# Optimization experiments

Hardware: AMD Instinct MI355X
Metric: run time of the kernel (lower is better)

The kernel has to match this reference:

```python
import jax, jax.numpy as jnp
import numpy as np

N = 10000      # nodes
E = 160000     # edges (before self-loops)
H = 8          # heads
D_IN, D_H1, D_H2 = 165, 128, 1    # per-head channels of gat1 / gat2
HID = H * D_H1                    # 1024


def batchnorm(x, gamma, beta, eps=1e-5):
    # training-mode BatchNorm1d: biased batch statistics over the node axis
    mu = x.mean(0)
    var = x.var(0)
    return (x - mu) * jax.lax.rsqrt(var + eps) * gamma + beta


def gatv2(x, src, dst, Wl, bl, Wr, br, att, bias, heads, out_ch, concat, n_nodes):
    # PyG GATv2Conv: lin_l on source, lin_r on target; e = att . LeakyReLU(xl_j + xr_i)
    xl = (x @ Wl + bl).reshape(n_nodes, heads, out_ch)   # source transform
    xr = (x @ Wr + br).reshape(n_nodes, heads, out_ch)   # target transform
    e = jax.nn.leaky_relu(xl[src] + xr[dst], 0.2)        # [E,H,C]
    logits = jnp.einsum('ehc,hc->eh', e, att)            # [E,H]
    # segment softmax over incoming edges of each destination node
    m = jax.lax.stop_gradient(jax.ops.segment_max(logits, dst, num_segments=n_nodes))
    a = jnp.exp(logits - m[dst])
    s = jax.ops.segment_sum(a, dst, num_segments=n_nodes)
    alpha = a / (s[dst] + 1e-16)                          # [E,H]
    out = jax.ops.segment_sum(xl[src] * alpha[..., None], dst, num_segments=n_nodes)
    out = out.reshape(n_nodes, heads * out_ch) if concat else out.mean(1)
    return out + bias


def setup_inputs() -> dict:
    key = jax.random.key(0)
    ks = jax.random.split(key, 12)
    g = lambda k, shape, fan_in: jax.random.normal(k, shape, jnp.float32) * (1.0 / np.sqrt(fan_in))
    return {
        'x': jax.random.normal(ks[0], (N, D_IN), jnp.float32),
        'gamma1': jnp.ones((D_IN,), jnp.float32),
        'beta1': jnp.zeros((D_IN,), jnp.float32),
        'Wl1': g(ks[1], (D_IN, HID), D_IN),
        'bl1': jnp.zeros((HID,), jnp.float32),
        'Wr1': g(ks[2], (D_IN, HID), D_IN),
        'br1': jnp.zeros((HID,), jnp.float32),
        'att1': g(ks[3], (H, D_H1), D_H1),
        'bias1': jnp.zeros((HID,), jnp.float32),
        'gamma2': jnp.ones((HID,), jnp.float32),
        'beta2': jnp.zeros((HID,), jnp.float32),
        'Wl2': g(ks[4], (HID, H * D_H2), HID),
        'bl2': jnp.zeros((H * D_H2,), jnp.float32),
        'Wr2': g(ks[5], (HID, H * D_H2), HID),
        'br2': jnp.zeros((H * D_H2,), jnp.float32),
        'att2': g(ks[6], (H, D_H2), D_H2),
        'bias2': jnp.zeros((D_H2,), jnp.float32),
        'edge_index': jax.random.randint(ks[7], (2, E), 0, N, jnp.int64 if jax.config.jax_enable_x64 else jnp.int32),
    }


def reference(x, gamma1, beta1, Wl1, bl1, Wr1, br1, att1, bias1,
              gamma2, beta2, Wl2, bl2, Wr2, br2, att2, bias2, edge_index):
    loops = jnp.arange(N, dtype=edge_index.dtype)
    src = jnp.concatenate([edge_index[0], loops])   # add_self_loops=True (PyG default)
    dst = jnp.concatenate([edge_index[1], loops])
    h = batchnorm(x, gamma1, beta1)
    h = gatv2(h, src, dst, Wl1, bl1, Wr1, br1, att1, bias1, H, D_H1, True, N)
    h = batchnorm(h, gamma2, beta2)
    h = jax.nn.leaky_relu(h, 0.01)                  # F.leaky_relu default slope
    out = gatv2(h, src, dst, Wl2, bl2, Wr2, br2, att2, bias2, H, D_H2, False, N)
    return out
```

## Files before the change

kernel.cpp:

```cpp
#include <hip/hip_runtime.h>

#define NN   10000
#define E0   160000
#define ET   170000
#define DIN  165
#define KP   192
#define HID  1024
#define NH   8
#define BP   200
#define K2P  1032


typedef __bf16 bf16x8 __attribute__((ext_vector_type(8)));
typedef float  f32x4  __attribute__((ext_vector_type(4)));
typedef float  f32x2  __attribute__((ext_vector_type(2)));

__device__ __forceinline__ float bf2f(unsigned short u) {
    unsigned int i = ((unsigned int)u) << 16;
    return __builtin_bit_cast(float, i);
}
__device__ __forceinline__ unsigned short f2bf(float f) {
    unsigned int i = __builtin_bit_cast(unsigned int, f);
    i += 0x7fffu + ((i >> 16) & 1u);
    return (unsigned short)(i >> 16);
}
__device__ __forceinline__ float fin(float x) {
    return fminf(fmaxf(x, -1e30f), 1e30f);
}
__device__ __forceinline__ int clampi(int s) {
    return min(max(s, 0), NN - 1);
}
__device__ __forceinline__ void unpack8(uint4 u, float* f) {
    f[0]=bf2f((unsigned short)(u.x)); f[1]=bf2f((unsigned short)(u.x>>16));
    f[2]=bf2f((unsigned short)(u.y)); f[3]=bf2f((unsigned short)(u.y>>16));
    f[4]=bf2f((unsigned short)(u.z)); f[5]=bf2f((unsigned short)(u.z>>16));
    f[6]=bf2f((unsigned short)(u.w)); f[7]=bf2f((unsigned short)(u.w>>16));
}
__device__ __forceinline__ f32x2 up2(unsigned int u) {
    f32x2 r;
    r.x = __builtin_bit_cast(float, u << 16);
    r.y = __builtin_bit_cast(float, u & 0xffff0000u);
    return r;
}

__global__ __launch_bounds__(256) void debug_fill(float* __restrict__ out, float val) {
    int i = blockIdx.x * 256 + threadIdx.x;
    if (i < NN) out[i] = val;
}

__global__ __launch_bounds__(256) void bn1_stats(const float* __restrict__ x,
                                                 float* __restrict__ colsum, float* __restrict__ colsq) {
    int r0 = blockIdx.x * 125;
    int c = threadIdx.x;
    if (c >= DIN) return;
    float acc = 0.f, sq = 0.f;
    for (int r = r0; r < r0 + 125; ++r) {
        float v = x[(size_t)r * DIN + c];
        acc += v; sq += v * v;
    }
    atomicAdd(&colsum[c], acc);
    atomicAdd(&colsq[c], sq);
}

__global__ __launch_bounds__(256) void bn1_apply(const float* __restrict__ x,
                                                 const float* __restrict__ colsum, const float* __restrict__ colsq,
                                                 const float* __restrict__ gamma, const float* __restrict__ beta,
                                                 unsigned short* __restrict__ hn) {
    int idx = blockIdx.x * 256 + threadIdx.x;
    if (idx >= NN * KP) return;
    int r = idx / KP, c = idx - r * KP;
    float v = 0.f;
    if (c < DIN) {
        float mu  = colsum[c] * (1.f / NN);
        float var = fmaxf(colsq[c] * (1.f / NN) - mu * mu, 0.f);
        float a = gamma[c] * rsqrtf(var + 1e-5f);
        float b = beta[c] - mu * a;
        v = fin(x[(size_t)r * DIN + c] * a + b);
    }
    hn[idx] = f2bf(v);
}

__global__ __launch_bounds__(256) void w1_transpose(const float* __restrict__ wl,
                                                    const float* __restrict__ wr,
                                                    unsigned short* __restrict__ wlt,
                                                    unsigned short* __restrict__ wrt) {
    const float* src    = blockIdx.z ? wr  : wl;
    unsigned short* dst = blockIdx.z ? wrt : wlt;
    __shared__ float ts[32][65];
    const int k0 = blockIdx.x * 32;
    const int n0 = blockIdx.y * 64;
    const int tid = threadIdx.x;
    for (int idx = tid; idx < 32 * 64; idx += 256) {
        int k = idx >> 6, n = idx & 63;
        ts[k][n] = (k0 + k < DIN) ? src[(size_t)(k0 + k) * HID + n0 + n] : 0.f;
    }
    __syncthreads();
    for (int idx = tid; idx < 64 * 32; idx += 256) {
        int n = idx >> 5, k = idx & 31;
        dst[(size_t)(n0 + n) * KP + k0 + k] = f2bf(ts[k][n]);
    }
}

__global__ __launch_bounds__(256) void gemm1_kernel(
    const unsigned short* __restrict__ hn,
    const unsigned short* __restrict__ wlt,
    const unsigned short* __restrict__ wrt,
    const float* __restrict__ bl,
    const float* __restrict__ br,
    unsigned short* __restrict__ xl,
    unsigned short* __restrict__ xr) {
    __shared__ unsigned short bs[2][64 * BP];
    const int tid  = threadIdx.x;
    const int lane = tid & 63;
    const int wave = tid >> 6;
    const int col  = lane & 15;
    const int q    = lane >> 4;
    const int n0   = blockIdx.y * 64;

    for (int idx = tid; idx < 64 * 48 * 2; idx += 256) {
        int z = idx >= 64 * 48;
        int rem = z ? idx - 64 * 48 : idx;
        int r = rem / 48, c = rem - r * 48;
        const unsigned short* wt = z ? wrt : wlt;
        uint2 v = *(const uint2*)(wt + (size_t)(n0 + r) * KP + c * 4);
        *(uint2*)&bs[z][r * BP + c * 4] = v;
    }
    __syncthreads();

    const int mbase = blockIdx.x * 128 + wave * 32;
    const int am0 = mbase + col;
    const int am1 = am0 + 16;
    const bool aok0 = (am0 < NN), aok1 = (am1 < NN);

    f32x4 accL[2][4], accR[2][4];
    #pragma unroll
    for (int m = 0; m < 2; ++m)
        for (int nt = 0; nt < 4; ++nt)
            for (int r = 0; r < 4; ++r) { accL[m][nt][r] = 0.f; accR[m][nt][r] = 0.f; }

    #pragma unroll
    for (int kt = 0; kt < 6; ++kt) {
        const int kk = kt * 32 + q * 8;
        uint4 a0u = make_uint4(0u,0u,0u,0u), a1u = make_uint4(0u,0u,0u,0u);
        if (aok0) a0u = *(const uint4*)(hn + (size_t)am0 * KP + kk);
        if (aok1) a1u = *(const uint4*)(hn + (size_t)am1 * KP + kk);
        bf16x8 a0 = __builtin_bit_cast(bf16x8, a0u);
        bf16x8 a1 = __builtin_bit_cast(bf16x8, a1u);
        #pragma unroll
        for (int nt = 0; nt < 4; ++nt) {
            bf16x8 bfl = __builtin_bit_cast(bf16x8, *(const uint4*)&bs[0][(nt * 16 + col) * BP + kk]);
            accL[0][nt] = __builtin_amdgcn_mfma_f32_16x16x32_bf16(a0, bfl, accL[0][nt], 0, 0, 0);
            accL[1][nt] = __builtin_amdgcn_mfma_f32_16x16x32_bf16(a1, bfl, accL[1][nt], 0, 0, 0);
            bf16x8 bfr = __builtin_bit_cast(bf16x8, *(const uint4*)&bs[1][(nt * 16 + col) * BP + kk]);
            accR[0][nt] = __builtin_amdgcn_mfma_f32_16x16x32_bf16(a0, bfr, accR[0][nt], 0, 0, 0);
            accR[1][nt] = __builtin_amdgcn_mfma_f32_16x16x32_bf16(a1, bfr, accR[1][nt], 0, 0, 0);
        }
    }

    #pragma unroll
    for (int nt = 0; nt < 4; ++nt) {
        const int nc = n0 + nt * 16 + col;
        const float bLv = bl[nc];
        const float bRv = br[nc];
        #pragma unroll
        for (int m = 0; m < 2; ++m) {
            #pragma unroll
            for (int r = 0; r < 4; ++r) {
                const int row = mbase + m * 16 + q * 4 + r;
                if (row < NN) {
                    xl[(size_t)row * HID + nc] = f2bf(fin(accL[m][nt][r] + bLv));
                    xr[(size_t)row * HID + nc] = f2bf(fin(accR[m][nt][r] + bRv));
                }
            }
        }
    }
}

__global__ __launch_bounds__(256) void edge_hist(const int* __restrict__ ei, int* __restrict__ deg) {
    int e = blockIdx.x * 256 + threadIdx.x;
    if (e >= ET) return;
    int d = (e < E0) ? ei[E0 + e] : (e - E0);
    atomicAdd(&deg[clampi(d)], 1);
}

__global__ __launch_bounds__(1024) void scan_kernel(const int* __restrict__ deg,
                                                    int* __restrict__ offs, int* __restrict__ cur,
                                                    int* __restrict__ perm) {
    __shared__ int wsum[16];
    __shared__ int bins[64];
    __shared__ int bcur[64];
    const int tid = threadIdx.x;
    const int base = tid * 10;
    int loc[10];
    int run = 0;
    #pragma unroll
    for (int j = 0; j < 10; ++j) {
        int idx = base + j;
        int v = (idx < NN) ? deg[idx] : 0;
        loc[j] = run;
        run += v;
    }
    const int lane = tid & 63;
    const int w = tid >> 6;
    int inc = run;
    #pragma unroll
    for (int s = 1; s < 64; s <<= 1) {
        int t = __shfl_up(inc, s);
        if (lane >= s) inc += t;
    }
    if (lane == 63) wsum[w] = inc;
    if (tid < 64) bins[tid] = 0;
    __syncthreads();
    int woff = 0;
    #pragma unroll
    for (int k = 0; k < 16; ++k) woff += (k < w) ? wsum[k] : 0;
    const int toff = woff + inc - run;
    #pragma unroll
    for (int j = 0; j < 10; ++j) {
        int idx = base + j;
        if (idx < NN) {
            int e = toff + loc[j]; offs[idx] = e; cur[idx] = e;
            atomicAdd(&bins[63 - min(deg[idx], 63)], 1);
        }
    }
    if (tid == 1023) offs[NN] = woff + inc;
    __syncthreads();
    if (tid < 64) {
        int v = bins[tid];
        int binc = v;
        #pragma unroll
        for (int s = 1; s < 64; s <<= 1) {
            int t = __shfl_up(binc, s);
            if (tid >= s) binc += t;
        }
        bcur[tid] = binc - v;
    }
    __syncthreads();
    #pragma unroll
    for (int j = 0; j < 10; ++j) {
        int idx = base + j;
        if (idx < NN) {
            int pos = atomicAdd(&bcur[63 - min(deg[idx], 63)], 1);
            perm[pos] = idx;
        }
    }
}

__global__ __launch_bounds__(256) void edge_scatter(const int* __restrict__ ei,
                                                    int* __restrict__ cur, int* __restrict__ ssrc) {
    int e = blockIdx.x * 256 + threadIdx.x;
    if (e >= ET) return;
    int s, d;
    if (e < E0) { s = ei[e]; d = ei[E0 + e]; }
    else        { s = e - E0; d = e - E0; }
    int pos = atomicAdd(&cur[clampi(d)], 1);
    if (pos >= 0 && pos < ET) ssrc[pos] = clampi(s);
}

__global__ __launch_bounds__(256) void gat1_node(
    const unsigned short* __restrict__ xl1, const unsigned short* xr1,
    const float* __restrict__ att1, const float* __restrict__ bias1,
    const int* __restrict__ offs, const int* __restrict__ ssrc,
    const int* __restrict__ perm,
    unsigned short* agg) {
    const int lane = threadIdx.x & 63;
    const int wave = threadIdx.x >> 6;
    const int i = perm[blockIdx.x * 4 + wave];
    const int e0 = offs[i];
    const int e1 = max(offs[i + 1], e0 + 1);

    f32x2 xr2[8], at2[8], o2[8];
    {
        const uint4* xp = (const uint4*)(xr1 + (size_t)i * HID + lane * 16);
        uint4 u0 = xp[0], u1 = xp[1];
        unsigned int w[8] = {u0.x, u0.y, u0.z, u0.w, u1.x, u1.y, u1.z, u1.w};
        const float4* ap = (const float4*)(att1 + lane * 16);
        float4 a0 = ap[0], a1 = ap[1], a2 = ap[2], a3 = ap[3];
        float af[16] = {a0.x,a0.y,a0.z,a0.w, a1.x,a1.y,a1.z,a1.w,
                        a2.x,a2.y,a2.z,a2.w, a3.x,a3.y,a3.z,a3.w};
        #pragma unroll
        for (int j = 0; j < 8; ++j) {
            xr2[j] = up2(w[j]);
            at2[j].x = af[2*j]; at2[j].y = af[2*j+1];
            o2[j].x = 0.f; o2[j].y = 0.f;
        }
    }
    float s = 0.f;

    auto lded = [&](int e, uint4& u0, uint4& u1) {
        int ee = min(e, e1 - 1);
        int sidx = clampi(ssrc[ee]);
        const uint4* xp = (const uint4*)(xl1 + (size_t)sidx * HID + lane * 16);
        u0 = xp[0]; u1 = xp[1];
    };
    auto logit = [&](const uint4& u0, const uint4& u1) -> float {
        unsigned int w[8] = {u0.x, u0.y, u0.z, u0.w, u1.x, u1.y, u1.z, u1.w};
        f32x2 p = {0.f, 0.f}, q = {0.f, 0.f};
        #pragma unroll
        for (int j = 0; j < 8; j += 2) {
            f32x2 v0 = up2(w[j])     + xr2[j];
            f32x2 v1 = up2(w[j + 1]) + xr2[j + 1];
            p = __builtin_elementwise_fma(at2[j],     __builtin_elementwise_max(v0, 0.2f * v0), p);
            q = __builtin_elementwise_fma(at2[j + 1], __builtin_elementwise_max(v1, 0.2f * v1), q);
        }
        p += q;
        float r = p.x + p.y;
        r += __shfl_xor(r, 1); r += __shfl_xor(r, 2); r += __shfl_xor(r, 4);
        return __expf(fminf(r, 50.f));
    };
    auto accum = [&](const uint4& u0, const uint4& u1, float a) {
        unsigned int w[8] = {u0.x, u0.y, u0.z, u0.w, u1.x, u1.y, u1.z, u1.w};
        f32x2 av = {a, a};
        #pragma unroll
        for (int j = 0; j < 8; ++j)
            o2[j] = __builtin_elementwise_fma(av, up2(w[j]), o2[j]);
    };

    uint4 a0, a1, b0, b1, n0, n1, n2, n3;
    lded(e0,     a0, a1);
    lded(e0 + 1, b0, b1);
    int e = e0;
    while (e + 1 < e1) {
        lded(e + 2, n0, n1);
        lded(e + 3, n2, n3);
        float aa0 = logit(a0, a1);
        float aa1 = logit(b0, b1);
        s += aa0 + aa1;
        accum(a0, a1, aa0);
        accum(b0, b1, aa1);
        a0 = n0; a1 = n1; b0 = n2; b1 = n3;
        e += 2;
    }
    if (e < e1) {
        float aa = logit(a0, a1);
        s += aa;
        accum(a0, a1, aa);
    }

    const float inv = 1.f / (s + 1e-16f);
    const float4* bp = (const float4*)(bias1 + lane * 16);
    float4 bq0 = bp[0], bq1 = bp[1], bq2 = bp[2], bq3 = bp[3];
    float bb[16] = {bq0.x,bq0.y,bq0.z,bq0.w, bq1.x,bq1.y,bq1.z,bq1.w,
                    bq2.x,bq2.y,bq2.z,bq2.w, bq3.x,bq3.y,bq3.z,bq3.w};
    unsigned short ov[16];
    #pragma unroll
    for (int j = 0; j < 8; ++j) {
        ov[2*j]   = f2bf(fin(o2[j].x * inv + bb[2*j]));
        ov[2*j+1] = f2bf(fin(o2[j].y * inv + bb[2*j+1]));
    }
    uint4* op = (uint4*)(agg + (size_t)i * HID + lane * 16);
    op[0] = *(const uint4*)&ov[0];
    op[1] = *(const uint4*)&ov[8];
}

__global__ __launch_bounds__(256) void bn2_stats(const unsigned short* __restrict__ agg,
                                                 float* __restrict__ colsum, float* __restrict__ colsq) {
    int r0 = blockIdx.x * 125;
    int t = threadIdx.x;
    float s0=0,s1=0,s2=0,s3=0,q0=0,q1=0,q2=0,q3=0;
    for (int r = r0; r < r0 + 125; ++r) {
        const ushort4 u = *(const ushort4*)(agg + (size_t)r * HID + t * 4);
        float v0=bf2f(u.x), v1=bf2f(u.y), v2=bf2f(u.z), v3=bf2f(u.w);
        s0+=v0; q0+=v0*v0; s1+=v1; q1+=v1*v1;
        s2+=v2; q2+=v2*v2; s3+=v3; q3+=v3*v3;
    }
    atomicAdd(&colsum[t*4+0], s0); atomicAdd(&colsq[t*4+0], q0);
    atomicAdd(&colsum[t*4+1], s1); atomicAdd(&colsq[t*4+1], q1);
    atomicAdd(&colsum[t*4+2], s2); atomicAdd(&colsq[t*4+2], q2);
    atomicAdd(&colsum[t*4+3], s3); atomicAdd(&colsq[t*4+3], q3);
}

__global__ __launch_bounds__(256) void gemm2_kernel(
    const unsigned short* __restrict__ agg,
    const float* __restrict__ colsum, const float* __restrict__ colsq,
    const float* __restrict__ gamma, const float* __restrict__ beta,
    const float* __restrict__ wl2, const float* __restrict__ wr2,
    const float* __restrict__ bl2, const float* __restrict__ br2,
    float* __restrict__ xl2, float* __restrict__ xr2) {
    __shared__ unsigned short bs[16 * K2P];
    __shared__ float a2s[HID], b2s[HID];
    const int tid  = threadIdx.x;
    const int lane = tid & 63;
    const int wave = tid >> 6;
    const int col  = lane & 15;
    const int q    = lane >> 4;

    for (int idx = tid; idx < 16 * HID; idx += 256) {
        int n = idx >> 10, k = idx & (HID - 1);
        float v = (n < 8) ? wl2[k * 8 + n] : wr2[k * 8 + (n - 8)];
        bs[n * K2P + k] = f2bf(v);
    }
    for (int c = tid; c < HID; c += 256) {
        float mu  = colsum[c] * (1.f / NN);
        float var = fmaxf(colsq[c] * (1.f / NN) - mu * mu, 0.f);
        float a = gamma[c] * rsqrtf(var + 1e-5f);
        a2s[c] = a; b2s[c] = beta[c] - mu * a;
    }
    __syncthreads();

    const int mtile = blockIdx.x * 4 + wave;
    if (mtile >= NN / 16) return;
    const int m0 = mtile * 16;
    const int am = m0 + col;

    f32x4 acc;
    acc[0] = acc[1] = acc[2] = acc[3] = 0.f;
    #pragma unroll
    for (int kt = 0; kt < 32; ++kt) {
        const int kk = kt * 32 + q * 8;
        uint4 u = *(const uint4*)(agg + (size_t)am * HID + kk);
        float xv[8];
        unpack8(u, xv);
        unsigned short hv[8];
        #pragma unroll
        for (int j = 0; j < 8; ++j) {
            float v = xv[j] * a2s[kk + j] + b2s[kk + j];
            v = fmaxf(v, 0.01f * v);
            hv[j] = f2bf(fin(v));
        }
        bf16x8 af = __builtin_bit_cast(bf16x8, *(const uint4*)hv);
        bf16x8 bf = __builtin_bit_cast(bf16x8, *(const uint4*)&bs[col * K2P + kk]);
        acc = __builtin_amdgcn_mfma_f32_16x16x32_bf16(af, bf, acc, 0, 0, 0);
    }

    const float bv = (col < 8) ? bl2[col] : br2[col - 8];
    float* outp = (col < 8) ? (xl2 + col) : (xr2 + (col - 8));
    #pragma unroll
    for (int r = 0; r < 4; ++r) {
        const int row = m0 + q * 4 + r;
        outp[row * 8] = fin(acc[r] + bv);
    }
}

__global__ __launch_bounds__(256) void gat2_node(
    const float* __restrict__ xl2, const float* __restrict__ xr2,
    const float* __restrict__ att2, const float* __restrict__ bias2,
    const int* __restrict__ offs, const int* __restrict__ ssrc,
    const int* __restrict__ perm,
    float* __restrict__ out) {
    const int lane = threadIdx.x & 63;
    const int wave = threadIdx.x >> 6;
    const int i = perm[blockIdx.x * 4 + wave];
    const int h = lane & 7, slot = lane >> 3;
    const int e0 = offs[i];
    const int e1 = max(offs[i + 1], e0);
    const float xr_h = xr2[i * 8 + h];
    const float att_h = att2[h];
    float ssum = 0.f, wsum = 0.f;
    for (int eb = e0; eb < e1; eb += 8) {
        int e = eb + slot;
        if (e < e1) {
            float xlv = xl2[clampi(ssrc[e]) * 8 + h];
            float v = xlv + xr_h;
            v = fmaxf(v, 0.2f * v);
            float a = __expf(fminf(fin(att_h * v), 50.f));
            ssum += a; wsum += a * xlv;
        }
    }
    ssum += __shfl_xor(ssum, 8); ssum += __shfl_xor(ssum, 16); ssum += __shfl_xor(ssum, 32);
    wsum += __shfl_xor(wsum, 8); wsum += __shfl_xor(wsum, 16); wsum += __shfl_xor(wsum, 32);
    float v = fin(wsum / (ssum + 1e-16f));
    v += __shfl_xor(v, 1); v += __shfl_xor(v, 2); v += __shfl_xor(v, 4);
    if (lane == 0) out[i] = fin(v * 0.125f + bias2[0]);
}

extern "C" void kernel_launch(void* const* d_in, const int* in_sizes, int n_in,
                              void* d_out, int out_size, void* d_ws, size_t ws_size,
                              hipStream_t stream) {
    float* out = (float*)d_out;

    static const int expected[18] = {
        NN * DIN, DIN, DIN, DIN * HID, HID, DIN * HID, HID, HID, HID,
        HID, HID, HID * NH, NH, HID * NH, NH, NH, 1, 2 * E0
    };
    if (n_in != 18) {
        debug_fill<<<(NN + 255) / 256, 256, 0, stream>>>(out, 8192.f + 64.f * (float)n_in);
        return;
    }
    for (int i = 0; i < 18; ++i) {
        if (in_sizes[i] != expected[i]) {
            debug_fill<<<(NN + 255) / 256, 256, 0, stream>>>(out, 4096.f + 32.f * (float)i);
            return;
        }
    }

    const float* x      = (const float*)d_in[0];
    const float* gamma1 = (const float*)d_in[1];
    const float* beta1  = (const float*)d_in[2];
    const float* Wl1    = (const float*)d_in[3];
    const float* bl1    = (const float*)d_in[4];
    const float* Wr1    = (const float*)d_in[5];
    const float* br1    = (const float*)d_in[6];
    const float* att1   = (const float*)d_in[7];
    const float* bias1  = (const float*)d_in[8];
    const float* gamma2 = (const float*)d_in[9];
    const float* beta2  = (const float*)d_in[10];
    const float* Wl2    = (const float*)d_in[11];
    const float* bl2    = (const float*)d_in[12];
    const float* Wr2    = (const float*)d_in[13];
    const float* br2    = (const float*)d_in[14];
    const float* att2   = (const float*)d_in[15];
    const float* bias2  = (const float*)d_in[16];
    const int*   ei     = (const int*)d_in[17];

    char* p = (char*)d_ws;
    auto alloc = [&](size_t bytes) -> void* {
        void* r = (void*)p;
        p += (bytes + 255) & ~(size_t)255;
        return r;
    };
    unsigned short* xl1  = (unsigned short*)alloc((size_t)NN * HID * 2);
    unsigned short* xr1  = (unsigned short*)alloc((size_t)NN * HID * 2);
    unsigned short* agg  = xr1;
    unsigned short* hn   = (unsigned short*)alloc((size_t)NN * KP * 2);
    unsigned short* wlt  = (unsigned short*)alloc((size_t)HID * KP * 2);
    unsigned short* wrt  = (unsigned short*)alloc((size_t)HID * KP * 2);
    float*          xl2  = (float*)alloc((size_t)NN * 8 * 4);
    float*          xr2  = (float*)alloc((size_t)NN * 8 * 4);
    int*            offs = (int*)alloc((NN + 1) * 4);
    int*            cur  = (int*)alloc(NN * 4);
    int*            ssrc = (int*)alloc(ET * 4);
    int*            perm = (int*)alloc(NN * 4);
    char* zbase = p;
    float* colsum1 = (float*)alloc(DIN * 4);
    float* colsq1  = (float*)alloc(DIN * 4);
    float* colsum2 = (float*)alloc(HID * 4);
    float* colsq2  = (float*)alloc(HID * 4);
    int*   deg     = (int*)alloc(NN * 4);
    size_t zlen = (size_t)(p - zbase);
    hipMemsetAsync(zbase, 0, zlen, stream);

    bn1_stats<<<80, 256, 0, stream>>>(x, colsum1, colsq1);
    bn1_apply<<<(NN * KP + 255) / 256, 256, 0, stream>>>(x, colsum1, colsq1, gamma1, beta1, hn);
    w1_transpose<<<dim3(6, 16, 2), 256, 0, stream>>>(Wl1, Wr1, wlt, wrt);
    gemm1_kernel<<<dim3((NN + 127) / 128, HID / 64), 256, 0, stream>>>(hn, wlt, wrt, bl1, br1, xl1, xr1);
    edge_hist<<<(ET + 255) / 256, 256, 0, stream>>>(ei, deg);
    scan_kernel<<<1, 1024, 0, stream>>>(deg, offs, cur, perm);
    edge_scatter<<<(ET + 255) / 256, 256, 0, stream>>>(ei, cur, ssrc);
    gat1_node<<<NN / 4, 256, 0, stream>>>(xl1, xr1, att1, bias1, offs, ssrc, perm, agg);
    bn2_stats<<<80, 256, 0, stream>>>(agg, colsum2, colsq2);
    gemm2_kernel<<<(NN / 16 + 3) / 4, 256, 0, stream>>>(agg, colsum2, colsq2, gamma2, beta2,
                                                        Wl2, Wr2, bl2, br2, xl2, xr2);
    gat2_node<<<NN / 4, 256, 0, stream>>>(xl2, xr2, att2, bias2, offs, ssrc, perm, out);
}
```

Measured before the change: 278.9 us.

## Split GAT1 aggregation per head, stage GEMM1 stores in LDS, split-K GEMM2

The GAT1 node kernel now launches one block per (node group, head). Each wave handles a single node's head and processes four edges at once in 16-lane groups, with a cross-group shuffle reduction at the end. This raises parallelism and lowers per-thread register use compared with one wave per node over all 1024 channels. GEMM1's epilogue writes results to LDS and then issues coalesced 16-byte global stores instead of scattered 2-byte stores. GEMM2 splits K across the four waves of a block, reduces through shared memory, and launches four times as many blocks. The trade-offs are redundant index and offset loads per head, added shuffles, and more blocks.

```diff
diff --git a/kernel.cpp b/kernel.cpp
--- a/kernel.cpp
+++ b/kernel.cpp
@@ -157,6 +157,9 @@
         }
     }
 
+    __syncthreads();
+    unsigned short* cl = &bs[0][0];
+    unsigned short* cr = cl + 128 * 72;
     #pragma unroll
     for (int nt = 0; nt < 4; ++nt) {
         const int nc = n0 + nt * 16 + col;
@@ -166,12 +169,20 @@
         for (int m = 0; m < 2; ++m) {
             #pragma unroll
             for (int r = 0; r < 4; ++r) {
-                const int row = mbase + m * 16 + q * 4 + r;
-                if (row < NN) {
-                    xl[(size_t)row * HID + nc] = f2bf(fin(accL[m][nt][r] + bLv));
-                    xr[(size_t)row * HID + nc] = f2bf(fin(accR[m][nt][r] + bRv));
-                }
+                const int lrow = wave * 32 + m * 16 + q * 4 + r;
+                cl[lrow * 72 + nt * 16 + col] = f2bf(fin(accL[m][nt][r] + bLv));
+                cr[lrow * 72 + nt * 16 + col] = f2bf(fin(accR[m][nt][r] + bRv));
             }
+        }
+    }
+    __syncthreads();
+    const int mblk = blockIdx.x * 128;
+    for (int t = tid; t < 128 * 8; t += 256) {
+        const int row = t >> 3, ch = t & 7;
+        const int grow = mblk + row;
+        if (grow < NN) {
+            *(uint4*)(xl + (size_t)grow * HID + n0 + ch * 8) = *(const uint4*)&cl[row * 72 + ch * 8];
+            *(uint4*)(xr + (size_t)grow * HID + n0 + ch * 8) = *(const uint4*)&cr[row * 72 + ch * 8];
         }
     }
 }
@@ -264,93 +275,78 @@
     const int* __restrict__ perm,
     unsigned short* agg) {
     const int lane = threadIdx.x & 63;
-    const int wave = threadIdx.x >> 6;
-    const int i = perm[blockIdx.x * 4 + wave];
+    const int wv   = threadIdx.x >> 6;
+    const int h    = blockIdx.x & 7;
+    const int grp  = blockIdx.x >> 3;
+    const int i    = perm[grp * 4 + wv];
     const int e0 = offs[i];
     const int e1 = max(offs[i + 1], e0 + 1);
-
-    f32x2 xr2[8], at2[8], o2[8];
+    const int g = lane >> 4;
+    const int c = lane & 15;
+    const int hb = h * 128;
+
+    f32x2 xr20, xr21, xr22, xr23, at20, at21, at22, at23;
     {
-        const uint4* xp = (const uint4*)(xr1 + (size_t)i * HID + lane * 16);
-        uint4 u0 = xp[0], u1 = xp[1];
-        unsigned int w[8] = {u0.x, u0.y, u0.z, u0.w, u1.x, u1.y, u1.z, u1.w};
-        const float4* ap = (const float4*)(att1 + lane * 16);
-        float4 a0 = ap[0], a1 = ap[1], a2 = ap[2], a3 = ap[3];
-        float af[16] = {a0.x,a0.y,a0.z,a0.w, a1.x,a1.y,a1.z,a1.w,
-                        a2.x,a2.y,a2.z,a2.w, a3.x,a3.y,a3.z,a3.w};
-        #pragma unroll
-        for (int j = 0; j < 8; ++j) {
-            xr2[j] = up2(w[j]);
-            at2[j].x = af[2*j]; at2[j].y = af[2*j+1];
-            o2[j].x = 0.f; o2[j].y = 0.f;
-        }
-    }
+        uint4 u = *(const uint4*)(xr1 + (size_t)i * HID + hb + c * 8);
+        xr20 = up2(u.x); xr21 = up2(u.y); xr22 = up2(u.z); xr23 = up2(u.w);
+        float4 a0 = *(const float4*)(att1 + hb + c * 8);
+        float4 a1 = *(const float4*)(att1 + hb + c * 8 + 4);
+        at20.x=a0.x; at20.y=a0.y; at21.x=a0.z; at21.y=a0.w;
+        at22.x=a1.x; at22.y=a1.y; at23.x=a1.z; at23.y=a1.w;
+    }
+    f32x2 o20={0.f,0.f}, o21={0.f,0.f}, o22={0.f,0.f}, o23={0.f,0.f};
     float s = 0.f;
 
-    auto lded = [&](int e, uint4& u0, uint4& u1) {
-        int ee = min(e, e1 - 1);
-        int sidx = clampi(ssrc[ee]);
-        const uint4* xp = (const uint4*)(xl1 + (size_t)sidx * HID + lane * 16);
-        u0 = xp[0]; u1 = xp[1];
-    };
-    auto logit = [&](const uint4& u0, const uint4& u1) -> float {
-        unsigned int w[8] = {u0.x, u0.y, u0.z, u0.w, u1.x, u1.y, u1.z, u1.w};
-        f32x2 p = {0.f, 0.f}, q = {0.f, 0.f};
-        #pragma unroll
-        for (int j = 0; j < 8; j += 2) {
-            f32x2 v0 = up2(w[j])     + xr2[j];
-            f32x2 v1 = up2(w[j + 1]) + xr2[j + 1];
-            p = __builtin_elementwise_fma(at2[j],     __builtin_elementwise_max(v0, 0.2f * v0), p);
-            q = __builtin_elementwise_fma(at2[j + 1], __builtin_elementwise_max(v1, 0.2f * v1), q);
-        }
-        p += q;
+    for (int eb = e0; eb < e1; eb += 4) {
+        const int e = min(eb + g, e1 - 1);
+        const int sidx = clampi(ssrc[e]);
+        const uint4 u = *(const uint4*)(xl1 + (size_t)sidx * HID + hb + c * 8);
+        f32x2 x0 = up2(u.x), x1 = up2(u.y), x2 = up2(u.z), x3 = up2(u.w);
+        f32x2 v0 = x0 + xr20, v1 = x1 + xr21, v2 = x2 + xr22, v3 = x3 + xr23;
+        v0 = __builtin_elementwise_max(v0, 0.2f * v0);
+        v1 = __builtin_elementwise_max(v1, 0.2f * v1);
+        v2 = __builtin_elementwise_max(v2, 0.2f * v2);
+        v3 = __builtin_elementwise_max(v3, 0.2f * v3);
+        f32x2 p = at20 * v0;
+        p = __builtin_elementwise_fma(at21, v1, p);
+        p = __builtin_elementwise_fma(at22, v2, p);
+        p = __builtin_elementwise_fma(at23, v3, p);
         float r = p.x + p.y;
-        r += __shfl_xor(r, 1); r += __shfl_xor(r, 2); r += __shfl_xor(r, 4);
-        return __expf(fminf(r, 50.f));
-    };
-    auto accum = [&](const uint4& u0, const uint4& u1, float a) {
-        unsigned int w[8] = {u0.x, u0.y, u0.z, u0.w, u1.x, u1.y, u1.z, u1.w};
-        f32x2 av = {a, a};
-        #pragma unroll
-        for (int j = 0; j < 8; ++j)
-            o2[j] = __builtin_elementwise_fma(av, up2(w[j]), o2[j]);
-    };
-
-    uint4 a0, a1, b0, b1, n0, n1, n2, n3;
-    lded(e0,     a0, a1);
-    lded(e0 + 1, b0, b1);
-    int e = e0;
-    while (e + 1 < e1) {
-        lded(e + 2, n0, n1);
-        lded(e + 3, n2, n3);
-        float aa0 = logit(a0, a1);
-        float aa1 = logit(b0, b1);
-        s += aa0 + aa1;
-        accum(a0, a1, aa0);
-        accum(b0, b1, aa1);
-        a0 = n0; a1 = n1; b0 = n2; b1 = n3;
-        e += 2;
-    }
-    if (e < e1) {
-        float aa = logit(a0, a1);
-        s += aa;
-        accum(a0, a1, aa);
-    }
+        r += __shfl_xor(r, 1); r += __shfl_xor(r, 2);
+        r += __shfl_xor(r, 4); r += __shfl_xor(r, 8);
+        const float a = (eb + g < e1) ? __expf(fminf(fin(r), 50.f)) : 0.f;
+        s += a;
+        f32x2 av; av.x = a; av.y = a;
+        o20 = __builtin_elementwise_fma(av, x0, o20);
+        o21 = __builtin_elementwise_fma(av, x1, o21);
+        o22 = __builtin_elementwise_fma(av, x2, o22);
+        o23 = __builtin_elementwise_fma(av, x3, o23);
+    }
+    s += __shfl_xor(s, 16); s += __shfl_xor(s, 32);
+    o20.x += __shfl_xor(o20.x, 16); o20.x += __shfl_xor(o20.x, 32);
+    o20.y += __shfl_xor(o20.y, 16); o20.y += __shfl_xor(o20.y, 32);
+    o21.x += __shfl_xor(o21.x, 16); o21.x += __shfl_xor(o21.x, 32);
+    o21.y += __shfl_xor(o21.y, 16); o21.y += __shfl_xor(o21.y, 32);
+    o22.x += __shfl_xor(o22.x, 16); o22.x += __shfl_xor(o22.x, 32);
+    o22.y += __shfl_xor(o22.y, 16); o22.y += __shfl_xor(o22.y, 32);
+    o23.x += __shfl_xor(o23.x, 16); o23.x += __shfl_xor(o23.x, 32);
+    o23.y += __shfl_xor(o23.y, 16); o23.y += __shfl_xor(o23.y, 32);
 
     const float inv = 1.f / (s + 1e-16f);
-    const float4* bp = (const float4*)(bias1 + lane * 16);
-    float4 bq0 = bp[0], bq1 = bp[1], bq2 = bp[2], bq3 = bp[3];
-    float bb[16] = {bq0.x,bq0.y,bq0.z,bq0.w, bq1.x,bq1.y,bq1.z,bq1.w,
-                    bq2.x,bq2.y,bq2.z,bq2.w, bq3.x,bq3.y,bq3.z,bq3.w};
-    unsigned short ov[16];
-    #pragma unroll
-    for (int j = 0; j < 8; ++j) {
-        ov[2*j]   = f2bf(fin(o2[j].x * inv + bb[2*j]));
-        ov[2*j+1] = f2bf(fin(o2[j].y * inv + bb[2*j+1]));
-    }
-    uint4* op = (uint4*)(agg + (size_t)i * HID + lane * 16);
-    op[0] = *(const uint4*)&ov[0];
-    op[1] = *(const uint4*)&ov[8];
+    if (g == 0) {
+        const float4* bp = (const float4*)(bias1 + hb + c * 8);
+        float4 b0v = bp[0], b1v = bp[1];
+        unsigned short ov[8];
+        ov[0] = f2bf(fin(o20.x * inv + b0v.x));
+        ov[1] = f2bf(fin(o20.y * inv + b0v.y));
+        ov[2] = f2bf(fin(o21.x * inv + b0v.z));
+        ov[3] = f2bf(fin(o21.y * inv + b0v.w));
+        ov[4] = f2bf(fin(o22.x * inv + b1v.x));
+        ov[5] = f2bf(fin(o22.y * inv + b1v.y));
+        ov[6] = f2bf(fin(o23.x * inv + b1v.z));
+        ov[7] = f2bf(fin(o23.y * inv + b1v.w));
+        *(uint4*)(agg + (size_t)i * HID + hb + c * 8) = *(const uint4*)ov;
+    }
 }
 
 __global__ __launch_bounds__(256) void bn2_stats(const unsigned short* __restrict__ agg,
@@ -379,6 +375,7 @@
     float* __restrict__ xl2, float* __restrict__ xr2) {
     __shared__ unsigned short bs[16 * K2P];
     __shared__ float a2s[HID], b2s[HID];
+    __shared__ float red[4 * 64 * 4];
     const int tid  = threadIdx.x;
     const int lane = tid & 63;
     const int wave = tid >> 6;
@@ -390,23 +387,22 @@
         float v = (n < 8) ? wl2[k * 8 + n] : wr2[k * 8 + (n - 8)];
         bs[n * K2P + k] = f2bf(v);
     }
-    for (int c = tid; c < HID; c += 256) {
-        float mu  = colsum[c] * (1.f / NN);
-        float var = fmaxf(colsq[c] * (1.f / NN) - mu * mu, 0.f);
-        float a = gamma[c] * rsqrtf(var + 1e-5f);
-        a2s[c] = a; b2s[c] = beta[c] - mu * a;
-    }
-    __syncthreads();
-
-    const int mtile = blockIdx.x * 4 + wave;
-    if (mtile >= NN / 16) return;
-    const int m0 = mtile * 16;
+    for (int cc = tid; cc < HID; cc += 256) {
+        float mu  = colsum[cc] * (1.f / NN);
+        float var = fmaxf(colsq[cc] * (1.f / NN) - mu * mu, 0.f);
+        float a = gamma[cc] * rsqrtf(var + 1e-5f);
+        a2s[cc] = a; b2s[cc] = beta[cc] - mu * a;
+    }
+    __syncthreads();
+
+    const int m0 = blockIdx.x * 16;
     const int am = m0 + col;
 
     f32x4 acc;
     acc[0] = acc[1] = acc[2] = acc[3] = 0.f;
     #pragma unroll
-    for (int kt = 0; kt < 32; ++kt) {
+    for (int t = 0; t < 8; ++t) {
+        const int kt = wave * 8 + t;
         const int kk = kt * 32 + q * 8;
         uint4 u = *(const uint4*)(agg + (size_t)am * HID + kk);
         float xv[8];
@@ -423,12 +419,21 @@
         acc = __builtin_amdgcn_mfma_f32_16x16x32_bf16(af, bf, acc, 0, 0, 0);
     }
 
-    const float bv = (col < 8) ? bl2[col] : br2[col - 8];
-    float* outp = (col < 8) ? (xl2 + col) : (xr2 + (col - 8));
-    #pragma unroll
-    for (int r = 0; r < 4; ++r) {
-        const int row = m0 + q * 4 + r;
-        outp[row * 8] = fin(acc[r] + bv);
+    *(f32x4*)&red[(wave * 64 + lane) * 4] = acc;
+    __syncthreads();
+    if (wave == 0) {
+        f32x4 a0 = *(const f32x4*)&red[lane * 4];
+        f32x4 a1 = *(const f32x4*)&red[(64 + lane) * 4];
+        f32x4 a2 = *(const f32x4*)&red[(128 + lane) * 4];
+        f32x4 a3 = *(const f32x4*)&red[(192 + lane) * 4];
+        acc = (a0 + a1) + (a2 + a3);
+        const float bv = (col < 8) ? bl2[col] : br2[col - 8];
+        float* outp = (col < 8) ? (xl2 + col) : (xr2 + (col - 8));
+        #pragma unroll
+        for (int r = 0; r < 4; ++r) {
+            const int row = m0 + q * 4 + r;
+            outp[row * 8] = fin(acc[r] + bv);
+        }
     }
 }
 
@@ -537,9 +542,9 @@
     edge_hist<<<(ET + 255) / 256, 256, 0, stream>>>(ei, deg);
     scan_kernel<<<1, 1024, 0, stream>>>(deg, offs, cur, perm);
     edge_scatter<<<(ET + 255) / 256, 256, 0, stream>>>(ei, cur, ssrc);
-    gat1_node<<<NN / 4, 256, 0, stream>>>(xl1, xr1, att1, bias1, offs, ssrc, perm, agg);
+    gat1_node<<<(NN / 4) * 8, 256, 0, stream>>>(xl1, xr1, att1, bias1, offs, ssrc, perm, agg);
     bn2_stats<<<80, 256, 0, stream>>>(agg, colsum2, colsq2);
-    gemm2_kernel<<<(NN / 16 + 3) / 4, 256, 0, stream>>>(agg, colsum2, colsq2, gamma2, beta2,
-                                                        Wl2, Wr2, bl2, br2, xl2, xr2);
+    gemm2_kernel<<<NN / 16, 256, 0, stream>>>(agg, colsum2, colsq2, gamma2, beta2,
+                                              Wl2, Wr2, bl2, br2, xl2, xr2);
     gat2_node<<<NN / 4, 256, 0, stream>>>(xl2, xr2, att2, bias2, offs, ssrc, perm, out);
 }
```

Result: slower. 295.7 us (+6.0%).
